# Kernel tuning notes

Hardware: AMD Instinct MI355X
Metric: run time of the kernel (lower is better)

Reference implementation:

```python
import jax, jax.numpy as jnp
import numpy as np

D_MODEL = 512
D_FF = 2048
NUM_EXPERTS = 8
TOP_K = 2


def setup_inputs() -> dict:
    key = jax.random.key(0)
    ks = jax.random.split(key, 6)
    scale = 0.02
    x = jax.random.normal(ks[0], (4, 8192, D_MODEL), dtype=jnp.float32)
    gate_w = jax.random.normal(ks[1], (D_MODEL, NUM_EXPERTS), dtype=jnp.float32) * scale
    w1 = jax.random.normal(ks[2], (NUM_EXPERTS, D_MODEL, D_FF), dtype=jnp.float32) * scale
    b1 = jnp.zeros((NUM_EXPERTS, D_FF), dtype=jnp.float32)
    w2 = jax.random.normal(ks[3], (NUM_EXPERTS, D_FF, D_MODEL), dtype=jnp.float32) * scale
    b2 = jnp.zeros((NUM_EXPERTS, D_MODEL), dtype=jnp.float32)
    return {"x": x, "gate_w": gate_w, "w1": w1, "b1": b1, "w2": w2, "b2": b2}


def reference(x, gate_w, w1, b1, w2, b2):
    B, S, D = x.shape
    xt = x.reshape(-1, D)                                  # [T, D]
    logits = xt @ gate_w                                   # [T, E]
    probs = jax.nn.softmax(logits, axis=-1)
    top_p, top_i = jax.lax.top_k(probs, TOP_K)             # [T, K]
    top_p = top_p / jnp.sum(top_p, axis=-1, keepdims=True)
    # per-token combine weight for each expert: [T, E]
    w_te = jnp.sum(jax.nn.one_hot(top_i, NUM_EXPERTS, dtype=xt.dtype) * top_p[..., None], axis=1)
    out = jnp.zeros_like(xt)
    for e in range(NUM_EXPERTS):  # small fixed loop over experts
        h = jax.nn.gelu(xt @ w1[e] + b1[e], approximate=False)  # [T, d_ff]
        y = h @ w2[e] + b2[e]                                   # [T, D]
        out = out + w_te[:, e:e + 1] * y
    return out.reshape(B, S, D)
```

## Files before the change

kernel.cpp:

```cpp
#include <hip/hip_runtime.h>
#include <math.h>

#define T_TOK 32768
#define DM 512
#define DFF 2048
#define NE 8
#define MAXTILES 528

typedef __attribute__((ext_vector_type(8))) short short8;
typedef __attribute__((ext_vector_type(4))) float f32x4;

__device__ __forceinline__ unsigned int f2bf1(float f) {
  union { float f; unsigned int u; } x; x.f = f;
  return (x.u + 0x7fffu + ((x.u >> 16) & 1u)) >> 16;
}

#define GLOAD(src, dst) \
  __builtin_amdgcn_global_load_lds((const __attribute__((address_space(1))) unsigned int*)(src), \
                                   (__attribute__((address_space(3))) unsigned int*)(dst), 16, 0, 0)
#define WAITVM(N) asm volatile("s_waitcnt vmcnt(" #N ")" ::: "memory")
#define BARRIER() asm volatile("s_barrier" ::: "memory")

__global__ void tcvt_kernel(const float* __restrict__ src, unsigned short* __restrict__ dst,
                            int R, int C) {
  __shared__ float tile[32][33];
  int e = blockIdx.z;
  const float* s = src + (size_t)e * R * C;
  unsigned short* d = dst + (size_t)e * R * C;
  int c0 = blockIdx.x * 32, r0 = blockIdx.y * 32;
  int tx = threadIdx.x, ty = threadIdx.y;
#pragma unroll
  for (int i = 0; i < 4; ++i)
    tile[ty + i * 8][tx] = s[(size_t)(r0 + ty + i * 8) * C + c0 + tx];
  __syncthreads();
#pragma unroll
  for (int i = 0; i < 4; ++i)
    d[(size_t)(c0 + ty + i * 8) * R + r0 + tx] = (unsigned short)f2bf1(tile[tx][ty + i * 8]);
}

__global__ __launch_bounds__(1024) void gate_kernel(
    const float* __restrict__ x, const float* __restrict__ gw,
    int* __restrict__ cnt, int* __restrict__ tok, float* __restrict__ wgt,
    unsigned int* __restrict__ xb) {
  __shared__ int lcnt[NE];
  __shared__ int lbase[NE];
  __shared__ int wslot[16][2];
  __shared__ int winfo[16][2];
  __shared__ float wval[16][2];
  int tid = threadIdx.x;
  int wid = tid >> 6, lane = tid & 63;
  int t = blockIdx.x * 16 + wid;
  if (tid < NE) lcnt[tid] = 0;
  __syncthreads();

  float acc[NE];
#pragma unroll
  for (int e = 0; e < NE; ++e) acc[e] = 0.f;
  const float* xr = x + (size_t)t * DM;
  unsigned int* xbr = xb + (size_t)t * (DM / 2);
#pragma unroll
  for (int j = 0; j < 4; ++j) {
    int d0 = j * 128 + lane * 2;
    float2 xv = *(const float2*)(xr + d0);
    const float* g0 = gw + d0 * NE;
#pragma unroll
    for (int e = 0; e < NE; ++e) acc[e] += xv.x * g0[e] + xv.y * g0[NE + e];
    xbr[j * 64 + lane] = f2bf1(xv.x) | (f2bf1(xv.y) << 16);
  }
#pragma unroll
  for (int off = 32; off >= 1; off >>= 1) {
#pragma unroll
    for (int e = 0; e < NE; ++e) acc[e] += __shfl_xor(acc[e], off);
  }
  if (lane == 0) {
    int e0 = 0; float l0 = acc[0];
#pragma unroll
    for (int e = 1; e < NE; ++e) if (acc[e] > l0) { l0 = acc[e]; e0 = e; }
    int e1 = (e0 == 0) ? 1 : 0; float l1 = acc[e1];
#pragma unroll
    for (int e = 0; e < NE; ++e) if (e != e0 && acc[e] > l1) { l1 = acc[e]; e1 = e; }
    float w0 = 1.f / (1.f + expf(l1 - l0));
    winfo[wid][0] = e0; winfo[wid][1] = e1;
    wval[wid][0] = w0;  wval[wid][1] = 1.f - w0;
    wslot[wid][0] = atomicAdd(&lcnt[e0], 1);
    wslot[wid][1] = atomicAdd(&lcnt[e1], 1);
  }
  __syncthreads();
  if (tid < NE) lbase[tid] = atomicAdd(&cnt[tid * 64], lcnt[tid]);
  __syncthreads();
  if (lane == 0) {
    int e0 = winfo[wid][0], e1 = winfo[wid][1];
    int p0 = lbase[e0] + wslot[wid][0];
    int p1 = lbase[e1] + wslot[wid][1];
    tok[e0 * T_TOK + p0] = t; wgt[e0 * T_TOK + p0] = wval[wid][0];
    tok[e1 * T_TOK + p1] = t; wgt[e1 * T_TOK + p1] = wval[wid][1];
  }
}

__global__ void plan_kernel(const int* __restrict__ cnt, int* __restrict__ tile_base) {
  if (threadIdx.x == 0 && blockIdx.x == 0) {
    int tb = 0;
    for (int e = 0; e < NE; ++e) { tile_base[e] = tb; tb += (cnt[e * 64] + 127) >> 7; }
    tile_base[NE] = tb;
  }
}

__global__ __launch_bounds__(256) void gemm1_kernel(
    const unsigned int* __restrict__ xb, const unsigned short* __restrict__ w1t,
    const float* __restrict__ b1, const int* __restrict__ cnt,
    const int* __restrict__ tok, const int* __restrict__ tile_base,
    unsigned short* __restrict__ H, int tile_lo) {
  int nwg = (int)gridDim.x;
  int bid0 = (int)blockIdx.x;
  int bid = (bid0 & 7) * (nwg >> 3) + (bid0 >> 3);
  int nt = bid & 15;
  int gt = tile_lo + (bid >> 4);
  if (gt >= tile_base[NE]) return;
  int e = 0;
#pragma unroll
  for (int k = 0; k < NE - 1; ++k) e += (gt >= tile_base[k + 1]) ? 1 : 0;
  int tloc = gt - tile_base[e];
  int ce = cnt[e * 64];
  int m0 = tloc * 128;
  int n0 = nt * 128;

  __shared__ char Lds[3 * 16384];

  int tid = (int)threadIdx.x;
  int lane = tid & 63;
  int wid = tid >> 6;
  int wm = wid & 1, wn = wid >> 1;
  int fl = lane & 15, q = lane >> 4;
  int sxy = ((q ^ ((fl >> 1) & 3)) << 4);

  const int* tokg = tok + e * T_TOK;
  int r0 = tid >> 2, r1 = 64 + (tid >> 2);
  int sl = tid & 3;
  int ss0 = sl ^ ((r0 >> 1) & 3);
  int ss1 = sl ^ ((r1 >> 1) & 3);
  int t0 = tokg[min(m0 + r0, ce - 1)];
  int t1 = tokg[min(m0 + r1, ce - 1)];
  const char* asrc0 = (const char*)xb + (size_t)t0 * 1024 + ss0 * 16;
  const char* asrc1 = (const char*)xb + (size_t)t1 * 1024 + ss1 * 16;
  const char* bsrc0 = (const char*)w1t + ((size_t)e * DFF + n0 + r0) * 1024 + ss0 * 16;
  const char* bsrc1 = (const char*)w1t + ((size_t)e * DFF + n0 + r1) * 1024 + ss1 * 16;

  int aoff[4], boff[4];
#pragma unroll
  for (int i = 0; i < 4; ++i) {
    aoff[i] = (wm * 64 + i * 16 + fl) * 64 + sxy;
    boff[i] = 8192 + (wn * 64 + i * 16 + fl) * 64 + sxy;
  }

  f32x4 acc[4][4];
#pragma unroll
  for (int a = 0; a < 4; ++a)
#pragma unroll
    for (int b = 0; b < 4; ++b) acc[a][b] = (f32x4){0.f, 0.f, 0.f, 0.f};

#define STAGE1(bi, ti) do { \
    char* base_ = Lds + (bi) * 16384; size_t ko_ = (size_t)(ti) * 64; \
    GLOAD(asrc0 + ko_, base_ + tid * 16);        \
    GLOAD(asrc1 + ko_, base_ + 4096 + tid * 16); \
    GLOAD(bsrc0 + ko_, base_ + 8192 + tid * 16); \
    GLOAD(bsrc1 + ko_, base_ + 12288 + tid * 16); } while (0)

#define COMP1(bi) do { \
    const char* base_ = Lds + (bi) * 16384; \
    short8 a[4], b[4]; \
    _Pragma("unroll") for (int i = 0; i < 4; ++i) { \
      a[i] = *(const short8*)(base_ + aoff[i]); \
      b[i] = *(const short8*)(base_ + boff[i]); } \
    _Pragma("unroll") for (int mf = 0; mf < 4; ++mf) \
    _Pragma("unroll") for (int nf = 0; nf < 4; ++nf) \
      acc[mf][nf] = __builtin_amdgcn_mfma_f32_16x16x32_bf16(a[mf], b[nf], acc[mf][nf], 0, 0, 0); \
  } while (0)

  STAGE1(0, 0); STAGE1(1, 1);
#pragma unroll
  for (int t = 0; t < 14; ++t) {
    WAITVM(4);
    BARRIER();
    STAGE1((t + 2) % 3, t + 2);
    COMP1(t % 3);
  }
  WAITVM(4); BARRIER(); COMP1(14 % 3);
  WAITVM(0); BARRIER(); COMP1(15 % 3);
#undef STAGE1
#undef COMP1

  size_t hrow0 = (size_t)(gt - tile_lo) * 128;
#pragma unroll
  for (int nf = 0; nf < 4; ++nf) {
    float bias = b1[e * DFF + n0 + wn * 64 + nf * 16 + fl];
    int col = n0 + wn * 64 + nf * 16 + fl;
#pragma unroll
    for (int mf = 0; mf < 4; ++mf)
#pragma unroll
      for (int j = 0; j < 4; ++j) {
        int row = wm * 64 + mf * 16 + q * 4 + j;
        float v = acc[mf][nf][j] + bias;
        float u2 = v * (1.5957691216f + 0.0713548162f * v * v);
        float g = v / (1.f + __expf(-u2));
        H[(hrow0 + row) * DFF + col] = (unsigned short)f2bf1(g);
      }
  }
}

__global__ __launch_bounds__(256) void gemm2_kernel(
    const unsigned short* __restrict__ H, const unsigned short* __restrict__ w2t,
    const float* __restrict__ b2, const int* __restrict__ cnt,
    const int* __restrict__ tok, const float* __restrict__ wgt,
    const int* __restrict__ tile_base, float* __restrict__ out, int tile_lo) {
  int nwg = (int)gridDim.x;
  int bid0 = (int)blockIdx.x;
  int bid = (bid0 & 7) * (nwg >> 3) + (bid0 >> 3);
  int nt = bid & 3;
  int gt = tile_lo + (bid >> 2);
  if (gt >= tile_base[NE]) return;
  int e = 0;
#pragma unroll
  for (int k = 0; k < NE - 1; ++k) e += (gt >= tile_base[k + 1]) ? 1 : 0;
  int tloc = gt - tile_base[e];
  int ce = cnt[e * 64];
  int m0 = tloc * 128;
  int n0 = nt * 128;

  __shared__ char Lds[4 * 16384];

  int tid = (int)threadIdx.x;
  int lane = tid & 63;
  int wid = tid >> 6;
  int wm = wid & 1, wn = wid >> 1;
  int fl = lane & 15, q = lane >> 4;
  int sxy = ((q ^ ((fl >> 1) & 3)) << 4);

  int r0 = tid >> 2, r1 = 64 + (tid >> 2);
  int sl = tid & 3;
  int ss0 = sl ^ ((r0 >> 1) & 3);
  int ss1 = sl ^ ((r1 >> 1) & 3);
  size_t hrow0 = (size_t)(gt - tile_lo) * 128;
  const char* asrc0 = (const char*)H + (hrow0 + r0) * 4096 + ss0 * 16;
  const char* asrc1 = (const char*)H + (hrow0 + r1) * 4096 + ss1 * 16;
  const char* bsrc0 = (const char*)w2t + ((size_t)e * DM + n0 + r0) * 4096 + ss0 * 16;
  const char* bsrc1 = (const char*)w2t + ((size_t)e * DM + n0 + r1) * 4096 + ss1 * 16;

  int aoff[4], boff[4];
#pragma unroll
  for (int i = 0; i < 4; ++i) {
    aoff[i] = (wm * 64 + i * 16 + fl) * 64 + sxy;
    boff[i] = 8192 + (wn * 64 + i * 16 + fl) * 64 + sxy;
  }

  f32x4 acc[4][4];
#pragma unroll
  for (int a = 0; a < 4; ++a)
#pragma unroll
    for (int b = 0; b < 4; ++b) acc[a][b] = (f32x4){0.f, 0.f, 0.f, 0.f};

#define STAGE2(bi, ti) do { \
    char* base_ = Lds + (bi) * 16384; size_t ko_ = (size_t)(ti) * 64; \
    GLOAD(asrc0 + ko_, base_ + tid * 16);        \
    GLOAD(asrc1 + ko_, base_ + 4096 + tid * 16); \
    GLOAD(bsrc0 + ko_, base_ + 8192 + tid * 16); \
    GLOAD(bsrc1 + ko_, base_ + 12288 + tid * 16); } while (0)

#define COMP2(bi) do { \
    const char* base_ = Lds + (bi) * 16384; \
    short8 a[4], b[4]; \
    _Pragma("unroll") for (int i = 0; i < 4; ++i) { \
      a[i] = *(const short8*)(base_ + aoff[i]); \
      b[i] = *(const short8*)(base_ + boff[i]); } \
    _Pragma("unroll") for (int mf = 0; mf < 4; ++mf) \
    _Pragma("unroll") for (int nf = 0; nf < 4; ++nf) \
      acc[mf][nf] = __builtin_amdgcn_mfma_f32_16x16x32_bf16(a[mf], b[nf], acc[mf][nf], 0, 0, 0); \
  } while (0)

#define STEP2(t, sb, cb) do { \
    WAITVM(8); BARRIER(); STAGE2(sb, (t) + 3); COMP2(cb); } while (0)

  STAGE2(0, 0); STAGE2(1, 1); STAGE2(2, 2);
  for (int tt = 0; tt < 60; tt += 4) {
    STEP2(tt + 0, 3, 0);
    STEP2(tt + 1, 0, 1);
    STEP2(tt + 2, 1, 2);
    STEP2(tt + 3, 2, 3);
  }
  WAITVM(8); BARRIER(); STAGE2(3, 63); COMP2(0);
  WAITVM(8); BARRIER(); COMP2(1);
  WAITVM(4); BARRIER(); COMP2(2);
  WAITVM(0); BARRIER(); COMP2(3);
#undef STEP2
#undef STAGE2
#undef COMP2

  const int* tokg = tok + e * T_TOK;
  const float* wgtg = wgt + e * T_TOK;
  float bias2[4];
#pragma unroll
  for (int nf = 0; nf < 4; ++nf) bias2[nf] = b2[e * DM + n0 + wn * 64 + nf * 16 + fl];
#pragma unroll
  for (int mf = 0; mf < 4; ++mf)
#pragma unroll
    for (int j = 0; j < 4; ++j) {
      int row = wm * 64 + mf * 16 + q * 4 + j;
      int slot = m0 + row;
      if (slot < ce) {
        int tk = tokg[slot];
        float w = wgtg[slot];
        float* orow = out + (size_t)tk * DM + n0 + wn * 64;
#pragma unroll
        for (int nf = 0; nf < 4; ++nf)
          atomicAdd(orow + nf * 16 + fl, w * (acc[mf][nf][j] + bias2[nf]));
      }
    }
}

extern "C" void kernel_launch(void* const* d_in, const int* in_sizes, int n_in,
                              void* d_out, int out_size, void* d_ws, size_t ws_size,
                              hipStream_t stream) {
  (void)in_sizes; (void)n_in; (void)out_size;
  const float* x  = (const float*)d_in[0];
  const float* gw = (const float*)d_in[1];
  const float* w1 = (const float*)d_in[2];
  const float* b1 = (const float*)d_in[3];
  const float* w2 = (const float*)d_in[4];
  const float* b2 = (const float*)d_in[5];
  float* out = (float*)d_out;

  char* ws = (char*)d_ws;
  size_t off = 0;
  auto alloc = [&](size_t sz) { char* p = ws + off; off += (sz + 255) & ~(size_t)255; return p; };
  int*   cnt = (int*)alloc(NE * 64 * 4);
  int*   tok = (int*)alloc((size_t)NE * T_TOK * 4);
  float* wgt = (float*)alloc((size_t)NE * T_TOK * 4);
  int*   tile_base = (int*)alloc((NE + 1) * 4);
  unsigned int* xb = (unsigned int*)alloc((size_t)T_TOK * (DM / 2) * 4);
  unsigned short* w1t = (unsigned short*)alloc((size_t)NE * DFF * DM * 2);
  unsigned short* w2t = (unsigned short*)alloc((size_t)NE * DM * DFF * 2);

  size_t avail = (ws_size > off) ? (ws_size - off) : 0;
  int TPC = MAXTILES, NC = 1;
  while (NC < 32 && (size_t)TPC * 128 * DFF * 2 > avail) {
    NC *= 2;
    TPC = (((MAXTILES + NC - 1) / NC) + 1) & ~1;
  }
  unsigned short* H = (unsigned short*)alloc((size_t)TPC * 128 * DFF * 2);

  hipMemsetAsync(cnt, 0, NE * 64 * 4, stream);
  hipMemsetAsync(out, 0, (size_t)T_TOK * DM * 4, stream);

  tcvt_kernel<<<dim3(DFF / 32, DM / 32, NE), dim3(32, 8), 0, stream>>>(w1, w1t, DM, DFF);
  tcvt_kernel<<<dim3(DM / 32, DFF / 32, NE), dim3(32, 8), 0, stream>>>(w2, w2t, DFF, DM);
  gate_kernel<<<T_TOK / 16, 1024, 0, stream>>>(x, gw, cnt, tok, wgt, xb);
  plan_kernel<<<1, 64, 0, stream>>>(cnt, tile_base);

  for (int c = 0; c * TPC < MAXTILES; ++c) {
    int lo = c * TPC;
    gemm1_kernel<<<TPC * 16, 256, 0, stream>>>(xb, w1t, b1, cnt, tok, tile_base, H, lo);
    gemm2_kernel<<<TPC * 4, 256, 0, stream>>>(H, w2t, b2, cnt, tok, wgt, tile_base, out, lo);
  }
}
```

Before: 600.8 us.

## Deepen gemm1 pipeline, pack H stores via permuted w2 layout, raise MFMA priority

gemm1 moves from a 3-buffer to a 4-buffer LDS pipeline with three tiles in flight, matching gemm2. Both GEMMs raise wave priority around their MFMA blocks with s_setprio. The GELU epilogue now writes two bf16 values per 32-bit store. To keep the result correct, the H column order inside each 32-column group is interleaved, and the w2 transpose applies the same permutation to its K dimension. The larger LDS footprint in gemm1 (64KB) may lower occupancy.

Result: faster. 582.4 us (-3.1%).

```diff
diff --git a/kernel.cpp b/kernel.cpp
--- a/kernel.cpp
+++ b/kernel.cpp
@@ -21,6 +21,7 @@
 #define WAITVM(N) asm volatile("s_waitcnt vmcnt(" #N ")" ::: "memory")
 #define BARRIER() asm volatile("s_barrier" ::: "memory")
 
+template <int PERM>
 __global__ void tcvt_kernel(const float* __restrict__ src, unsigned short* __restrict__ dst,
                             int R, int C) {
   __shared__ float tile[32][33];
@@ -34,8 +35,11 @@
     tile[ty + i * 8][tx] = s[(size_t)(r0 + ty + i * 8) * C + c0 + tx];
   __syncthreads();
 #pragma unroll
-  for (int i = 0; i < 4; ++i)
-    d[(size_t)(c0 + ty + i * 8) * R + r0 + tx] = (unsigned short)f2bf1(tile[tx][ty + i * 8]);
+  for (int i = 0; i < 4; ++i) {
+    int rr = r0 + tx;
+    if (PERM) rr = (rr & ~31) | ((rr & 15) << 1) | ((rr >> 4) & 1);
+    d[(size_t)(c0 + ty + i * 8) * R + rr] = (unsigned short)f2bf1(tile[tx][ty + i * 8]);
+  }
 }
 
 __global__ __launch_bounds__(1024) void gate_kernel(
@@ -124,7 +128,7 @@
   int m0 = tloc * 128;
   int n0 = nt * 128;
 
-  __shared__ char Lds[3 * 16384];
+  __shared__ char Lds[4 * 16384];
 
   int tid = (int)threadIdx.x;
   int lane = tid & 63;
@@ -171,40 +175,51 @@
     _Pragma("unroll") for (int i = 0; i < 4; ++i) { \
       a[i] = *(const short8*)(base_ + aoff[i]); \
       b[i] = *(const short8*)(base_ + boff[i]); } \
+    __builtin_amdgcn_s_setprio(1); \
     _Pragma("unroll") for (int mf = 0; mf < 4; ++mf) \
     _Pragma("unroll") for (int nf = 0; nf < 4; ++nf) \
       acc[mf][nf] = __builtin_amdgcn_mfma_f32_16x16x32_bf16(a[mf], b[nf], acc[mf][nf], 0, 0, 0); \
+    __builtin_amdgcn_s_setprio(0); \
   } while (0)
 
-  STAGE1(0, 0); STAGE1(1, 1);
-#pragma unroll
-  for (int t = 0; t < 14; ++t) {
-    WAITVM(4);
-    BARRIER();
-    STAGE1((t + 2) % 3, t + 2);
-    COMP1(t % 3);
-  }
-  WAITVM(4); BARRIER(); COMP1(14 % 3);
-  WAITVM(0); BARRIER(); COMP1(15 % 3);
+#define STEP1(t, sb, cb) do { \
+    WAITVM(8); BARRIER(); STAGE1(sb, (t) + 3); COMP1(cb); } while (0)
+
+  STAGE1(0, 0); STAGE1(1, 1); STAGE1(2, 2);
+  for (int tt = 0; tt < 12; tt += 4) {
+    STEP1(tt + 0, 3, 0);
+    STEP1(tt + 1, 0, 1);
+    STEP1(tt + 2, 1, 2);
+    STEP1(tt + 3, 2, 3);
+  }
+  WAITVM(8); BARRIER(); STAGE1(3, 15); COMP1(0);
+  WAITVM(8); BARRIER(); COMP1(1);
+  WAITVM(4); BARRIER(); COMP1(2);
+  WAITVM(0); BARRIER(); COMP1(3);
+#undef STEP1
 #undef STAGE1
 #undef COMP1
 
   size_t hrow0 = (size_t)(gt - tile_lo) * 128;
-#pragma unroll
-  for (int nf = 0; nf < 4; ++nf) {
-    float bias = b1[e * DFF + n0 + wn * 64 + nf * 16 + fl];
-    int col = n0 + wn * 64 + nf * 16 + fl;
-#pragma unroll
-    for (int mf = 0; mf < 4; ++mf)
-#pragma unroll
-      for (int j = 0; j < 4; ++j) {
-        int row = wm * 64 + mf * 16 + q * 4 + j;
-        float v = acc[mf][nf][j] + bias;
+  float bv[4];
+#pragma unroll
+  for (int nf = 0; nf < 4; ++nf) bv[nf] = b1[e * DFF + n0 + wn * 64 + nf * 16 + fl];
+#pragma unroll
+  for (int mf = 0; mf < 4; ++mf)
+#pragma unroll
+    for (int j = 0; j < 4; ++j) {
+      int row = wm * 64 + mf * 16 + q * 4 + j;
+      float g[4];
+#pragma unroll
+      for (int nf = 0; nf < 4; ++nf) {
+        float v = acc[mf][nf][j] + bv[nf];
         float u2 = v * (1.5957691216f + 0.0713548162f * v * v);
-        float g = v / (1.f + __expf(-u2));
-        H[(hrow0 + row) * DFF + col] = (unsigned short)f2bf1(g);
+        g[nf] = v / (1.f + __expf(-u2));
       }
-  }
+      unsigned int* Hp = (unsigned int*)(H + (hrow0 + row) * DFF + n0 + wn * 64);
+      Hp[fl]      = f2bf1(g[0]) | (f2bf1(g[1]) << 16);
+      Hp[16 + fl] = f2bf1(g[2]) | (f2bf1(g[3]) << 16);
+    }
 }
 
 __global__ __launch_bounds__(256) void gemm2_kernel(
@@ -271,9 +286,11 @@
     _Pragma("unroll") for (int i = 0; i < 4; ++i) { \
       a[i] = *(const short8*)(base_ + aoff[i]); \
       b[i] = *(const short8*)(base_ + boff[i]); } \
+    __builtin_amdgcn_s_setprio(1); \
     _Pragma("unroll") for (int mf = 0; mf < 4; ++mf) \
     _Pragma("unroll") for (int nf = 0; nf < 4; ++nf) \
       acc[mf][nf] = __builtin_amdgcn_mfma_f32_16x16x32_bf16(a[mf], b[nf], acc[mf][nf], 0, 0, 0); \
+    __builtin_amdgcn_s_setprio(0); \
   } while (0)
 
 #define STEP2(t, sb, cb) do { \
@@ -350,8 +367,8 @@
   hipMemsetAsync(cnt, 0, NE * 64 * 4, stream);
   hipMemsetAsync(out, 0, (size_t)T_TOK * DM * 4, stream);
 
-  tcvt_kernel<<<dim3(DFF / 32, DM / 32, NE), dim3(32, 8), 0, stream>>>(w1, w1t, DM, DFF);
-  tcvt_kernel<<<dim3(DM / 32, DFF / 32, NE), dim3(32, 8), 0, stream>>>(w2, w2t, DFF, DM);
+  tcvt_kernel<0><<<dim3(DFF / 32, DM / 32, NE), dim3(32, 8), 0, stream>>>(w1, w1t, DM, DFF);
+  tcvt_kernel<1><<<dim3(DM / 32, DFF / 32, NE), dim3(32, 8), 0, stream>>>(w2, w2t, DFF, DM);
   gate_kernel<<<T_TOK / 16, 1024, 0, stream>>>(x, gw, cnt, tok, wgt, xb);
   plan_kernel<<<1, 64, 0, stream>>>(cnt, tile_base);
 
```
